# Performance work log

Hardware: AMD Instinct MI355X
Metric: run time of the kernel (lower is better)

Reference implementation:

```python
import jax, jax.numpy as jnp
import numpy as np

NUM_CLASSES = 5
TRANSITION_PENALTY = 0.1
SMOOTHING = 0.1


def _make_transition_matrix(c: int) -> jnp.ndarray:
    i = np.arange(c)[:, None]
    j = np.arange(c)[None, :]
    d = np.abs(i - j)
    t = np.where(d == 0, 0.0, np.where(d == 1, 0.5, np.where(d == 2, 1.0, 2.0)))
    return jnp.asarray(t, dtype=jnp.float32)


def setup_inputs() -> dict:
    key = jax.random.key(0)
    k1, k2 = jax.random.split(key)
    B = 4194304
    inputs = jax.random.normal(k1, (B, NUM_CLASSES), dtype=jnp.float32)
    targets = jax.random.randint(k2, (B,), 0, NUM_CLASSES, dtype=jnp.int32)
    return {"inputs": inputs, "targets": targets}


def reference(inputs, targets):
    c = NUM_CLASSES
    log_probs = jax.nn.log_softmax(inputs, axis=-1)  # [B, C]
    # label-smoothing CE: smooth target dist has (1-s) on target, s/(C-1) elsewhere
    onehot = jax.nn.one_hot(targets, c, dtype=log_probs.dtype)
    smooth = SMOOTHING / (c - 1)
    smooth_targets = onehot * (1.0 - SMOOTHING - smooth) + smooth
    ce_loss = (-(smooth_targets * log_probs).sum(axis=-1)).mean()
    # transition penalty: mean_i sum_j softmax(inputs)[i,j] * T[targets[i], j]
    probs = jnp.exp(log_probs)
    T = _make_transition_matrix(c)
    penalty = (probs * T[targets]).sum(axis=-1).mean()
    return ce_loss + TRANSITION_PENALTY * penalty
```

## Files before the change

kernel.cpp:

```cpp
#include <hip/hip_runtime.h>


constexpr int C = 5;
constexpr int BLOCK = 256;
constexpr int ROWS_PER_TILE = 4 * BLOCK;
constexpr int F4_PER_TILE = ROWS_PER_TILE * C / 4;

__device__ __forceinline__ float trans_w(int d) {
    d = d < 0 ? -d : d;
    return (d >= 3) ? 2.0f : 0.5f * (float)d;
}

__device__ __forceinline__ float row_loss(float a0, float a1, float a2,
                                          float a3, float a4, int t) {
    float m = fmaxf(fmaxf(fmaxf(a0, a1), fmaxf(a2, a3)), a4);
    float e0 = __expf(a0 - m);
    float e1 = __expf(a1 - m);
    float e2 = __expf(a2 - m);
    float e3 = __expf(a3 - m);
    float e4 = __expf(a4 - m);
    float s  = e0 + e1 + e2 + e3 + e4;
    float ls = __logf(s);
    float inv = 1.0f / s;

    float lp0 = a0 - m - ls;
    float lp1 = a1 - m - ls;
    float lp2 = a2 - m - ls;
    float lp3 = a3 - m - ls;
    float lp4 = a4 - m - ls;
    float sumlp = lp0 + lp1 + lp2 + lp3 + lp4;
    float lpt = (t == 0) ? lp0 : (t == 1) ? lp1 : (t == 2) ? lp2
              : (t == 3) ? lp3 : lp4;

    float pen = e0 * trans_w(t)     + e1 * trans_w(t - 1) + e2 * trans_w(t - 2)
              + e3 * trans_w(t - 3) + e4 * trans_w(t - 4);
    pen *= inv;

    return -(0.875f * lpt + 0.025f * sumlp) + 0.1f * pen;
}

__global__ __launch_bounds__(BLOCK) void bloom_partial(
        const float* __restrict__ x, const int* __restrict__ tgt,
        double* __restrict__ partial, int nTiles, int B) {
    __shared__ float4 tile4[F4_PER_TILE];
    __shared__ double wsum[4];

    const int tid = threadIdx.x;
    const int tile = blockIdx.x;
    float local = 0.0f;

    if (tile < nTiles) {
        const float4* __restrict__ x4 = (const float4*)x;
        const long base4 = (long)tile * F4_PER_TILE;
        float4 v0 = x4[base4 + 0 * BLOCK + tid];
        float4 v1 = x4[base4 + 1 * BLOCK + tid];
        float4 v2 = x4[base4 + 2 * BLOCK + tid];
        float4 v3 = x4[base4 + 3 * BLOCK + tid];
        float4 v4 = x4[base4 + 4 * BLOCK + tid];
        int4 t4 = ((const int4*)tgt)[(long)tile * BLOCK + tid];

        tile4[0 * BLOCK + tid] = v0;
        tile4[1 * BLOCK + tid] = v1;
        tile4[2 * BLOCK + tid] = v2;
        tile4[3 * BLOCK + tid] = v3;
        tile4[4 * BLOCK + tid] = v4;
        __syncthreads();

        float4 r0 = tile4[tid * 5 + 0];
        float4 r1 = tile4[tid * 5 + 1];
        float4 r2 = tile4[tid * 5 + 2];
        float4 r3 = tile4[tid * 5 + 3];
        float4 r4 = tile4[tid * 5 + 4];

        local  = row_loss(r0.x, r0.y, r0.z, r0.w, r1.x, t4.x);
        local += row_loss(r1.y, r1.z, r1.w, r2.x, r2.y, t4.y);
        local += row_loss(r2.z, r2.w, r3.x, r3.y, r3.z, t4.z);
        local += row_loss(r3.w, r4.x, r4.y, r4.z, r4.w, t4.w);
    }

    if (blockIdx.x == gridDim.x - 1) {
        for (int r = nTiles * ROWS_PER_TILE + tid; r < B; r += BLOCK) {
            local += row_loss(x[(long)r * C + 0], x[(long)r * C + 1],
                              x[(long)r * C + 2], x[(long)r * C + 3],
                              x[(long)r * C + 4], tgt[r]);
        }
    }

    #pragma unroll
    for (int off = 32; off > 0; off >>= 1)
        local += __shfl_down(local, off, 64);
    const int lane = tid & 63;
    const int wid = tid >> 6;
    if (lane == 0) wsum[wid] = (double)local;
    __syncthreads();
    if (tid == 0)
        partial[blockIdx.x] = wsum[0] + wsum[1] + wsum[2] + wsum[3];
}

__global__ __launch_bounds__(BLOCK) void bloom_final(
        const double* __restrict__ partial, float* __restrict__ out,
        int nPartials, int B) {
    __shared__ double wsum[4];
    const int tid = threadIdx.x;
    double s = 0.0;
    for (int i = tid; i < nPartials; i += BLOCK)
        s += partial[i];
    #pragma unroll
    for (int off = 32; off > 0; off >>= 1)
        s += __shfl_down(s, off, 64);
    const int lane = tid & 63;
    const int wid = tid >> 6;
    if (lane == 0) wsum[wid] = s;
    __syncthreads();
    if (tid == 0)
        out[0] = (float)((wsum[0] + wsum[1] + wsum[2] + wsum[3]) / (double)B);
}

extern "C" void kernel_launch(void* const* d_in, const int* in_sizes, int n_in,
                              void* d_out, int out_size, void* d_ws, size_t ws_size,
                              hipStream_t stream) {
    const float* x = (const float*)d_in[0];
    const int* tgt = (const int*)d_in[1];
    float* out = (float*)d_out;

    int B = in_sizes[1];
    int nTiles = B / ROWS_PER_TILE;
    int blocks = (nTiles > 0) ? nTiles : 1;

    double* partial = (double*)d_ws;

    bloom_partial<<<blocks, BLOCK, 0, stream>>>(x, tgt, partial, nTiles, B);
    bloom_final<<<1, BLOCK, 0, stream>>>(partial, out, blocks, B);
}
```

Before: 138.4 us.

## Drop LDS transpose; load eight contiguous rows per thread directly

Removes the shared-memory staging tile and barrier: each thread now reads its 8 rows (ten float4 plus two int4) straight from global memory and computes the loss in registers. The aim is to cut LDS traffic and the sync, and to put more loads in flight per thread. The trade-off is that global loads become strided by 160 bytes across lanes instead of fully coalesced, and the grid shrinks to half as many blocks.

Measured after the change: 137.3 us. No clear change (-0.8%).

```diff
diff --git a/kernel.cpp b/kernel.cpp
--- a/kernel.cpp
+++ b/kernel.cpp
@@ -3,8 +3,8 @@
 
 constexpr int C = 5;
 constexpr int BLOCK = 256;
-constexpr int ROWS_PER_TILE = 4 * BLOCK;
-constexpr int F4_PER_TILE = ROWS_PER_TILE * C / 4;
+constexpr int ROWS_PER_THREAD = 8;
+constexpr int ROWS_PER_BLOCK = BLOCK * ROWS_PER_THREAD;
 
 __device__ __forceinline__ float trans_w(int d) {
     d = d < 0 ? -d : d;
@@ -39,47 +39,46 @@
     return -(0.875f * lpt + 0.025f * sumlp) + 0.1f * pen;
 }
 
+__device__ __forceinline__ float quad_loss(float4 v0, float4 v1, float4 v2,
+                                           float4 v3, float4 v4, int4 t) {
+    float r;
+    r  = row_loss(v0.x, v0.y, v0.z, v0.w, v1.x, t.x);
+    r += row_loss(v1.y, v1.z, v1.w, v2.x, v2.y, t.y);
+    r += row_loss(v2.z, v2.w, v3.x, v3.y, v3.z, t.z);
+    r += row_loss(v3.w, v4.x, v4.y, v4.z, v4.w, t.w);
+    return r;
+}
+
 __global__ __launch_bounds__(BLOCK) void bloom_partial(
         const float* __restrict__ x, const int* __restrict__ tgt,
-        double* __restrict__ partial, int nTiles, int B) {
-    __shared__ float4 tile4[F4_PER_TILE];
-    __shared__ double wsum[4];
-
+        double* __restrict__ partial, int nGroups, int B) {
     const int tid = threadIdx.x;
-    const int tile = blockIdx.x;
+    const int g = blockIdx.x * BLOCK + tid;
     float local = 0.0f;
 
-    if (tile < nTiles) {
+    if (g < nGroups) {
         const float4* __restrict__ x4 = (const float4*)x;
-        const long base4 = (long)tile * F4_PER_TILE;
-        float4 v0 = x4[base4 + 0 * BLOCK + tid];
-        float4 v1 = x4[base4 + 1 * BLOCK + tid];
-        float4 v2 = x4[base4 + 2 * BLOCK + tid];
-        float4 v3 = x4[base4 + 3 * BLOCK + tid];
-        float4 v4 = x4[base4 + 4 * BLOCK + tid];
-        int4 t4 = ((const int4*)tgt)[(long)tile * BLOCK + tid];
+        const int4* __restrict__ tgt4 = (const int4*)tgt;
+        const long b4 = (long)g * 10;
+        float4 v0 = x4[b4 + 0];
+        float4 v1 = x4[b4 + 1];
+        float4 v2 = x4[b4 + 2];
+        float4 v3 = x4[b4 + 3];
+        float4 v4 = x4[b4 + 4];
+        float4 v5 = x4[b4 + 5];
+        float4 v6 = x4[b4 + 6];
+        float4 v7 = x4[b4 + 7];
+        float4 v8 = x4[b4 + 8];
+        float4 v9 = x4[b4 + 9];
+        int4 ta = tgt4[(long)g * 2 + 0];
+        int4 tb = tgt4[(long)g * 2 + 1];
 
-        tile4[0 * BLOCK + tid] = v0;
-        tile4[1 * BLOCK + tid] = v1;
-        tile4[2 * BLOCK + tid] = v2;
-        tile4[3 * BLOCK + tid] = v3;
-        tile4[4 * BLOCK + tid] = v4;
-        __syncthreads();
-
-        float4 r0 = tile4[tid * 5 + 0];
-        float4 r1 = tile4[tid * 5 + 1];
-        float4 r2 = tile4[tid * 5 + 2];
-        float4 r3 = tile4[tid * 5 + 3];
-        float4 r4 = tile4[tid * 5 + 4];
-
-        local  = row_loss(r0.x, r0.y, r0.z, r0.w, r1.x, t4.x);
-        local += row_loss(r1.y, r1.z, r1.w, r2.x, r2.y, t4.y);
-        local += row_loss(r2.z, r2.w, r3.x, r3.y, r3.z, t4.z);
-        local += row_loss(r3.w, r4.x, r4.y, r4.z, r4.w, t4.w);
+        local  = quad_loss(v0, v1, v2, v3, v4, ta);
+        local += quad_loss(v5, v6, v7, v8, v9, tb);
     }
 
     if (blockIdx.x == gridDim.x - 1) {
-        for (int r = nTiles * ROWS_PER_TILE + tid; r < B; r += BLOCK) {
+        for (int r = nGroups * ROWS_PER_THREAD + tid; r < B; r += BLOCK) {
             local += row_loss(x[(long)r * C + 0], x[(long)r * C + 1],
                               x[(long)r * C + 2], x[(long)r * C + 3],
                               x[(long)r * C + 4], tgt[r]);
@@ -89,6 +88,7 @@
     #pragma unroll
     for (int off = 32; off > 0; off >>= 1)
         local += __shfl_down(local, off, 64);
+    __shared__ double wsum[4];
     const int lane = tid & 63;
     const int wid = tid >> 6;
     if (lane == 0) wsum[wid] = (double)local;
@@ -124,11 +124,12 @@
     float* out = (float*)d_out;
 
     int B = in_sizes[1];
-    int nTiles = B / ROWS_PER_TILE;
-    int blocks = (nTiles > 0) ? nTiles : 1;
+    int nGroups = B / ROWS_PER_THREAD;
+    int blocks = (nGroups + BLOCK - 1) / BLOCK;
+    if (blocks < 1) blocks = 1;
 
     double* partial = (double*)d_ws;
 
-    bloom_partial<<<blocks, BLOCK, 0, stream>>>(x, tgt, partial, nTiles, B);
+    bloom_partial<<<blocks, BLOCK, 0, stream>>>(x, tgt, partial, nGroups, B);
     bloom_final<<<1, BLOCK, 0, stream>>>(partial, out, blocks, B);
 }
```
